# Optimization experiments

Measured on AMD Instinct MI355X. Metric: run time of the kernel, lower is better.

Reference implementation:

```python
import jax, jax.numpy as jnp
import numpy as np

N, E = 50000, 800000
DIN, DOUT = 256, 128
DH = 2 * DOUT  # hidden width of conv1


def setup_inputs() -> dict:
    key = jax.random.key(0)
    ks = jax.random.split(key, 9)
    x = jax.random.normal(ks[0], (N, DIN), dtype=jnp.float32)
    edge_index = jax.random.randint(ks[1], (2, E), 0, N, dtype=jnp.int64)
    edge_weight = jax.random.uniform(ks[2], (E,), dtype=jnp.float32)
    s1 = 1.0 / np.sqrt(DIN)
    s2 = 1.0 / np.sqrt(DH)
    W1 = jax.random.uniform(ks[3], (DIN, DH), minval=-s1, maxval=s1, dtype=jnp.float32)
    b1 = jnp.zeros((DH,), jnp.float32)
    Wmu = jax.random.uniform(ks[4], (DH, DOUT), minval=-s2, maxval=s2, dtype=jnp.float32)
    bmu = jnp.zeros((DOUT,), jnp.float32)
    Wls = jax.random.uniform(ks[5], (DH, DOUT), minval=-s2, maxval=s2, dtype=jnp.float32)
    bls = jnp.zeros((DOUT,), jnp.float32)
    return {"x": x, "edge_index": edge_index, "edge_weight": edge_weight,
            "W1": W1, "b1": b1, "Wmu": Wmu, "bmu": bmu, "Wls": Wls, "bls": bls}


def _gcn_layer(x, row, col, norm, W, b, n):
    # GCNConv: linear transform, then normalized scatter-add aggregation, then bias
    h = x @ W                                   # [N, Dout]
    msg = h[row] * norm[:, None]                # gather source feats, scale per-edge
    agg = jax.ops.segment_sum(msg, col, num_segments=n)  # scatter-add to targets
    return agg + b


def reference(x, edge_index, edge_weight, W1, b1, Wmu, bmu, Wls, bls):
    n = x.shape[0]
    row, col = edge_index[0], edge_index[1]
    # add self loops with weight 1 (PyG gcn_norm default, fill_value=1)
    loop = jnp.arange(n)
    row_f = jnp.concatenate([row, loop])
    col_f = jnp.concatenate([col, loop])
    ew = jnp.concatenate([edge_weight, jnp.ones((n,), x.dtype)])
    # symmetric normalization: deg computed over destination index
    deg = jax.ops.segment_sum(ew, col_f, num_segments=n)
    dinv = jnp.where(deg > 0, jax.lax.rsqrt(deg), 0.0)
    norm = dinv[row_f] * ew * dinv[col_f]       # cached=True -> same norm each layer
    h = jax.nn.relu(_gcn_layer(x, row_f, col_f, norm, W1, b1, n))
    mu = _gcn_layer(h, row_f, col_f, norm, Wmu, bmu, n)
    logstd = _gcn_layer(h, row_f, col_f, norm, Wls, bls, n)
    return mu, logstd
```

## Files before the change

### kernel.cpp

```cpp
#include <hip/hip_runtime.h>
#include <hip/hip_fp16.h>

#define THREADS 256
#define DEG_SHIFT 44
#define DEG_SCALE 16777216.0f
#define DEG_MASK  ((1ULL << DEG_SHIFT) - 1)

typedef __attribute__((ext_vector_type(8))) short bf16x8;
typedef __attribute__((ext_vector_type(4))) float f32x4;
typedef __attribute__((ext_vector_type(8))) unsigned short u16x8;

__device__ inline float bf2f(unsigned short u) {
    union { unsigned int i; float f; } v; v.i = ((unsigned int)u) << 16; return v.f;
}
__device__ inline unsigned short f2bf(float f) {
    union { float f; unsigned int i; } v; v.f = f;
    unsigned int i = v.i;
    i += 0x7fff + ((i >> 16) & 1);
    return (unsigned short)(i >> 16);
}

__global__ void k_init(unsigned long long* __restrict__ packed, int n) {
    int i = blockIdx.x * THREADS + threadIdx.x;
    if (i < n) packed[i] = 0ULL;
}

__global__ void k_count(const int* __restrict__ dst, const float* __restrict__ ew,
                        unsigned long long* __restrict__ packed,
                        int* __restrict__ rank, int E) {
    int e = blockIdx.x * THREADS + threadIdx.x;
    if (e >= E) return;
    int c = dst[e];
    unsigned long long v = (1ULL << DEG_SHIFT) |
        (unsigned long long)(ew[e] * DEG_SCALE + 0.5f);
    unsigned long long old = atomicAdd(&packed[c], v);
    rank[e] = (int)(old >> DEG_SHIFT);
}

__global__ void k_unpack(const unsigned long long* __restrict__ packed,
                         int* __restrict__ counts, float* __restrict__ dinv, int n) {
    int i = blockIdx.x * THREADS + threadIdx.x;
    if (i >= n) return;
    unsigned long long p = packed[i];
    counts[i] = (int)(p >> DEG_SHIFT);
    float d = 1.0f + (float)(p & DEG_MASK) * (1.0f / DEG_SCALE);
    dinv[i] = rsqrtf(d);
}

__global__ void k_scan_part(const int* __restrict__ counts, int* __restrict__ offsets,
                            int* __restrict__ blocksum, int n) {
    __shared__ int s[THREADS];
    int i = blockIdx.x * THREADS + threadIdx.x;
    int v = (i < n) ? counts[i] : 0;
    s[threadIdx.x] = v;
    __syncthreads();
    for (int d = 1; d < THREADS; d <<= 1) {
        int t = (threadIdx.x >= d) ? s[threadIdx.x - d] : 0;
        __syncthreads();
        s[threadIdx.x] += t;
        __syncthreads();
    }
    if (i < n) offsets[i] = s[threadIdx.x] - v;
    if (threadIdx.x == THREADS - 1) blocksum[blockIdx.x] = s[THREADS - 1];
}

__global__ void k_scan_block(int* __restrict__ blocksum, int nb) {
    __shared__ int s[THREADS];
    int v = (threadIdx.x < nb) ? blocksum[threadIdx.x] : 0;
    s[threadIdx.x] = v;
    __syncthreads();
    for (int d = 1; d < THREADS; d <<= 1) {
        int t = (threadIdx.x >= d) ? s[threadIdx.x - d] : 0;
        __syncthreads();
        s[threadIdx.x] += t;
        __syncthreads();
    }
    if (threadIdx.x < nb) blocksum[threadIdx.x] = s[threadIdx.x] - v;
}

__global__ void k_scan_add(int* __restrict__ offsets, const int* __restrict__ blocksum,
                           const int* __restrict__ counts, int2* __restrict__ combo, int n) {
    int i = blockIdx.x * THREADS + threadIdx.x;
    if (i >= n) return;
    int o = offsets[i] + blocksum[blockIdx.x];
    offsets[i] = o;
    combo[i] = make_int2(o, counts[i]);
}

__global__ void k_fill(const int* __restrict__ ei, const float* __restrict__ ew,
                       const float* __restrict__ dinv, const int* __restrict__ offsets,
                       const int* __restrict__ rank, unsigned int* __restrict__ csr, int E) {
    int e = blockIdx.x * THREADS + threadIdx.x;
    if (e >= E) return;
    int r = ei[e];
    int c = ei[E + e];
    float nrm = dinv[r] * ew[e] * dinv[c];
    unsigned short h = __half_as_ushort(__float2half_rn(nrm));
    csr[offsets[c] + rank[e]] = ((unsigned int)r << 16) | h;
}

__global__ void k_cvt_w(const float* __restrict__ W1, const float* __restrict__ Wmu,
                        const float* __restrict__ Wls, const float* __restrict__ bmu,
                        const float* __restrict__ bls,
                        ushort* __restrict__ W1t, ushort* __restrict__ Wct,
                        float* __restrict__ bcat) {
    int n = blockIdx.x, k = threadIdx.x;
    if (n < 256) {
        W1t[n * 256 + k] = f2bf(W1[k * 256 + n]);
    } else if (n < 512) {
        int nn = n - 256;
        float v = (nn < 128) ? Wmu[k * 128 + nn] : Wls[k * 128 + (nn - 128)];
        Wct[nn * 256 + k] = f2bf(v);
    } else {
        bcat[k] = (k < 128) ? bmu[k] : bls[k - 128];
    }
}

template<int MODE>
__global__ __launch_bounds__(256) void k_agg(const ushort* __restrict__ fb,
        const int2* __restrict__ combo, const unsigned int* __restrict__ csr,
        const float* __restrict__ dinv, const float* __restrict__ bias,
        void* __restrict__ out, int n) {
    int slice = blockIdx.x & 7;
    int grp   = blockIdx.x >> 3;
    int wv = threadIdx.x >> 6, lane = threadIdx.x & 63;
    int n2 = lane >> 4;
    int g  = (lane >> 2) & 3;
    int c  = lane & 3;
    int col0 = slice * 32;

    float b8[8];
    {
        const float4* bp = (const float4*)(bias + col0 + c * 8);
        float4 b0 = bp[0], b1 = bp[1];
        b8[0] = b0.x; b8[1] = b0.y; b8[2] = b0.z; b8[3] = b0.w;
        b8[4] = b1.x; b8[5] = b1.y; b8[6] = b1.z; b8[7] = b1.w;
    }

    int node = grp * 16 + wv * 4 + n2;
    bool valid = node < n;
    int nid = valid ? node : 0;
    int2 oc = combo[nid];
    int off = oc.x, cnt = valid ? oc.y : 0;
    float di = dinv[nid];

    float acc[8] = {};
    if (g == 0 && valid) {
        u16x8 u = *(const u16x8*)(fb + (size_t)nid * 256 + col0 + c * 8);
        float s = di * di;
        #pragma unroll
        for (int k = 0; k < 8; k++) acc[k] = s * bf2f(u[k]);
    }

    int cmax = cnt;
    cmax = max(cmax, __shfl_xor(cmax, 16));
    cmax = max(cmax, __shfl_xor(cmax, 32));

    const unsigned int* row = csr + off;
    for (int e0 = 0; e0 < cmax; e0 += 4) {
        int e = e0 + g;
        unsigned int m = (e < cnt) ? row[e] : 0u;
        int src = (int)(m >> 16);
        float w = __half2float(__ushort_as_half((unsigned short)(m & 0xffffu)));
        u16x8 u = *(const u16x8*)(fb + (size_t)src * 256 + col0 + c * 8);
        #pragma unroll
        for (int k = 0; k < 8; k++) acc[k] += w * bf2f(u[k]);
    }

    #pragma unroll
    for (int k = 0; k < 8; k++) acc[k] += __shfl_xor(acc[k], 4);
    #pragma unroll
    for (int k = 0; k < 8; k++) acc[k] += __shfl_xor(acc[k], 8);

    if (g == 0 && valid) {
        #pragma unroll
        for (int k = 0; k < 8; k++) acc[k] += b8[k];
        if (MODE == 0) {
            u16x8 o;
            #pragma unroll
            for (int k = 0; k < 8; k++) o[k] = f2bf(fmaxf(acc[k], 0.f));
            *(u16x8*)((ushort*)out + (size_t)node * 256 + col0 + c * 8) = o;
        } else {
            float* mu = (float*)out;
            float* dst = (slice < 4)
                ? mu + (size_t)node * 128 + col0 + c * 8
                : mu + (size_t)n * 128 + (size_t)node * 128 + (col0 - 128) + c * 8;
            float4* d4 = (float4*)dst;
            float4 o0, o1;
            o0.x = acc[0]; o0.y = acc[1]; o0.z = acc[2]; o0.w = acc[3];
            o1.x = acc[4]; o1.y = acc[5]; o1.z = acc[6]; o1.w = acc[7];
            d4[0] = o0; d4[1] = o1;
        }
    }
}

#define LDT 40
template<int AF32>
__global__ __launch_bounds__(256) void k_gemm(const void* __restrict__ Ain,
        const ushort* __restrict__ Bt, ushort* __restrict__ C, int M) {
    __shared__ ushort As[128 * LDT];
    __shared__ ushort Bs[128 * LDT];
    const float*  Af = (const float*)Ain;
    const ushort* Ab = (const ushort*)Ain;
    int tid = threadIdx.x;
    int lane = tid & 63, wave = tid >> 6;
    int row0 = blockIdx.y * 128, col0 = blockIdx.x * 128;
    int mw = (wave >> 1) * 64, nw = (wave & 1) * 64;
    int lr = lane & 15, lq = lane >> 4;
    f32x4 acc[4][4] = {};
    for (int k0 = 0; k0 < 256; k0 += 32) {
        #pragma unroll
        for (int i = 0; i < 2; i++) {
            int cc = tid + i * 256;
            int r = cc >> 2, q = cc & 3;
            int gr = row0 + r;
            int4 av = make_int4(0, 0, 0, 0);
            if (gr < M) {
                if (AF32) {
                    const float* p = Af + (size_t)gr * 256 + k0 + q * 8;
                    float4 lo = *(const float4*)p;
                    float4 hi = *(const float4*)(p + 4);
                    ushort* u = (ushort*)&av;
                    u[0] = f2bf(lo.x); u[1] = f2bf(lo.y);
                    u[2] = f2bf(lo.z); u[3] = f2bf(lo.w);
                    u[4] = f2bf(hi.x); u[5] = f2bf(hi.y);
                    u[6] = f2bf(hi.z); u[7] = f2bf(hi.w);
                } else {
                    av = *(const int4*)(Ab + (size_t)gr * 256 + k0 + q * 8);
                }
            }
            *(int4*)(&As[r * LDT + q * 8]) = av;
            int4 bv = *(const int4*)(Bt + (size_t)(col0 + r) * 256 + k0 + q * 8);
            *(int4*)(&Bs[r * LDT + q * 8]) = bv;
        }
        __syncthreads();
        bf16x8 af[4], bfr[4];
        #pragma unroll
        for (int mi = 0; mi < 4; mi++)
            af[mi] = *(const bf16x8*)(&As[(mw + mi * 16 + lr) * LDT + lq * 8]);
        #pragma unroll
        for (int ni = 0; ni < 4; ni++)
            bfr[ni] = *(const bf16x8*)(&Bs[(nw + ni * 16 + lr) * LDT + lq * 8]);
        #pragma unroll
        for (int mi = 0; mi < 4; mi++)
            #pragma unroll
            for (int ni = 0; ni < 4; ni++)
                acc[mi][ni] = __builtin_amdgcn_mfma_f32_16x16x32_bf16(
                    af[mi], bfr[ni], acc[mi][ni], 0, 0, 0);
        __syncthreads();
    }
    #pragma unroll
    for (int mi = 0; mi < 4; mi++)
        #pragma unroll
        for (int ni = 0; ni < 4; ni++)
            #pragma unroll
            for (int r = 0; r < 4; r++) {
                int grow = row0 + mw + mi * 16 + lq * 4 + r;
                int gcol = col0 + nw + ni * 16 + lr;
                if (grow < M) C[(size_t)grow * 256 + gcol] = f2bf(acc[mi][ni][r]);
            }
}

extern "C" void kernel_launch(void* const* d_in, const int* in_sizes, int n_in,
                              void* d_out, int out_size, void* d_ws, size_t ws_size,
                              hipStream_t stream) {
    const float* x   = (const float*)d_in[0];
    const int*   ei  = (const int*)d_in[1];
    const float* ew  = (const float*)d_in[2];
    const float* W1  = (const float*)d_in[3];
    const float* b1  = (const float*)d_in[4];
    const float* Wmu = (const float*)d_in[5];
    const float* bmu = (const float*)d_in[6];
    const float* Wls = (const float*)d_in[7];
    const float* bls = (const float*)d_in[8];

    const int DIN = 256;
    const int N = in_sizes[0] / DIN;
    const int E = in_sizes[2];

    unsigned long long* packed = (unsigned long long*)d_ws;
    int*   counts   = (int*)(packed + N);
    int*   offsets  = counts + N;
    float* dinv     = (float*)(offsets + N);
    int2*  combo    = (int2*)(dinv + N);
    int*   blocksum = (int*)(combo + N);
    int*   rank     = blocksum + 256;
    unsigned int* csr = (unsigned int*)(rank + E);
    ushort* xw      = (ushort*)(csr + E);
    ushort* hb      = xw + (size_t)N * 256;
    ushort* hw      = hb + (size_t)N * 256;
    ushort* W1t     = hw + (size_t)N * 256;
    ushort* Wct     = W1t + 256 * 256;
    float*  bcat    = (float*)(Wct + 256 * 256);

    int gN = (N + THREADS - 1) / THREADS;
    int gE = (E + THREADS - 1) / THREADS;

    k_init<<<gN, THREADS, 0, stream>>>(packed, N);
    k_count<<<gE, THREADS, 0, stream>>>(ei + E, ew, packed, rank, E);
    k_unpack<<<gN, THREADS, 0, stream>>>(packed, counts, dinv, N);

    k_scan_part<<<gN, THREADS, 0, stream>>>(counts, offsets, blocksum, N);
    k_scan_block<<<1, THREADS, 0, stream>>>(blocksum, gN);
    k_scan_add<<<gN, THREADS, 0, stream>>>(offsets, blocksum, counts, combo, N);

    k_fill<<<gE, THREADS, 0, stream>>>(ei, ew, dinv, offsets, rank, csr, E);

    k_cvt_w<<<513, THREADS, 0, stream>>>(W1, Wmu, Wls, bmu, bls, W1t, Wct, bcat);

    int gAgg = 8 * ((N + 15) / 16);
    dim3 ggrid(2, (N + 127) / 128);

    k_gemm<1><<<ggrid, 256, 0, stream>>>(x, W1t, xw, N);
    k_agg<0><<<gAgg, THREADS, 0, stream>>>(xw, combo, csr, dinv, b1, hb, N);

    k_gemm<0><<<ggrid, 256, 0, stream>>>(hb, Wct, hw, N);
    k_agg<1><<<gAgg, THREADS, 0, stream>>>(hw, combo, csr, dinv, bcat, d_out, N);
}
```

Before: 396.6 us.

## Pad CSR rows to multiples of four and aggregate one node per wave

The exclusive scan now rounds each node's edge count up to a multiple of four, so every CSR row starts 16-byte aligned and can be read with a single uint4 load. The aggregation kernel is remapped so each wave handles one node over a 64-column slice: eight edge groups each process four preloaded edges, then a tail loop covers rows with more than 32 edges. Per-node loop divergence across wave lanes goes away, and the CSR index fetch becomes vectorized. In exchange, waves with fewer than 32 edges still issue masked gathers of row 0, cross-lane reductions grow to three shuffle stages, and the workspace grows to hold the padding.

```diff
diff --git a/kernel.cpp b/kernel.cpp
--- a/kernel.cpp
+++ b/kernel.cpp
@@ -51,7 +51,7 @@
                             int* __restrict__ blocksum, int n) {
     __shared__ int s[THREADS];
     int i = blockIdx.x * THREADS + threadIdx.x;
-    int v = (i < n) ? counts[i] : 0;
+    int v = (i < n) ? ((counts[i] + 3) & ~3) : 0;
     s[threadIdx.x] = v;
     __syncthreads();
     for (int d = 1; d < THREADS; d <<= 1) {
@@ -121,29 +121,23 @@
         const int2* __restrict__ combo, const unsigned int* __restrict__ csr,
         const float* __restrict__ dinv, const float* __restrict__ bias,
         void* __restrict__ out, int n) {
-    int slice = blockIdx.x & 7;
-    int grp   = blockIdx.x >> 3;
+    int slice = blockIdx.x & 3;
+    int grp   = blockIdx.x >> 2;
     int wv = threadIdx.x >> 6, lane = threadIdx.x & 63;
-    int n2 = lane >> 4;
-    int g  = (lane >> 2) & 3;
-    int c  = lane & 3;
-    int col0 = slice * 32;
-
-    float b8[8];
-    {
-        const float4* bp = (const float4*)(bias + col0 + c * 8);
-        float4 b0 = bp[0], b1 = bp[1];
-        b8[0] = b0.x; b8[1] = b0.y; b8[2] = b0.z; b8[3] = b0.w;
-        b8[4] = b1.x; b8[5] = b1.y; b8[6] = b1.z; b8[7] = b1.w;
-    }
-
-    int node = grp * 16 + wv * 4 + n2;
+    int g = lane >> 3;
+    int c = lane & 7;
+    int col0 = slice * 64;
+
+    int node = grp * 4 + wv;
     bool valid = node < n;
     int nid = valid ? node : 0;
     int2 oc = combo[nid];
     int off = oc.x, cnt = valid ? oc.y : 0;
     float di = dinv[nid];
 
+    const unsigned int* row = csr + off;
+    uint4 q = *(const uint4*)(row + 4 * g);
+
     float acc[8] = {};
     if (g == 0 && valid) {
         u16x8 u = *(const u16x8*)(fb + (size_t)nid * 256 + col0 + c * 8);
@@ -152,29 +146,44 @@
         for (int k = 0; k < 8; k++) acc[k] = s * bf2f(u[k]);
     }
 
-    int cmax = cnt;
-    cmax = max(cmax, __shfl_xor(cmax, 16));
-    cmax = max(cmax, __shfl_xor(cmax, 32));
-
-    const unsigned int* row = csr + off;
-    for (int e0 = 0; e0 < cmax; e0 += 4) {
-        int e = e0 + g;
-        unsigned int m = (e < cnt) ? row[e] : 0u;
-        int src = (int)(m >> 16);
-        float w = __half2float(__ushort_as_half((unsigned short)(m & 0xffffu)));
-        u16x8 u = *(const u16x8*)(fb + (size_t)src * 256 + col0 + c * 8);
-        #pragma unroll
-        for (int k = 0; k < 8; k++) acc[k] += w * bf2f(u[k]);
-    }
-
-    #pragma unroll
-    for (int k = 0; k < 8; k++) acc[k] += __shfl_xor(acc[k], 4);
+    {
+        unsigned int mm[4] = { q.x, q.y, q.z, q.w };
+        #pragma unroll
+        for (int j = 0; j < 4; j++) {
+            int e = 4 * g + j;
+            unsigned int m = (e < cnt) ? mm[j] : 0u;
+            int src = (int)(m >> 16);
+            float w = __half2float(__ushort_as_half((unsigned short)(m & 0xffffu)));
+            u16x8 u = *(const u16x8*)(fb + (size_t)src * 256 + col0 + c * 8);
+            #pragma unroll
+            for (int k = 0; k < 8; k++) acc[k] += w * bf2f(u[k]);
+        }
+    }
+    if (cnt > 32) {
+        for (int e0 = 32; e0 < cnt; e0 += 8) {
+            int e = e0 + g;
+            unsigned int m = (e < cnt) ? row[e] : 0u;
+            int src = (int)(m >> 16);
+            float w = __half2float(__ushort_as_half((unsigned short)(m & 0xffffu)));
+            u16x8 u = *(const u16x8*)(fb + (size_t)src * 256 + col0 + c * 8);
+            #pragma unroll
+            for (int k = 0; k < 8; k++) acc[k] += w * bf2f(u[k]);
+        }
+    }
+
     #pragma unroll
     for (int k = 0; k < 8; k++) acc[k] += __shfl_xor(acc[k], 8);
+    #pragma unroll
+    for (int k = 0; k < 8; k++) acc[k] += __shfl_xor(acc[k], 16);
+    #pragma unroll
+    for (int k = 0; k < 8; k++) acc[k] += __shfl_xor(acc[k], 32);
 
     if (g == 0 && valid) {
-        #pragma unroll
-        for (int k = 0; k < 8; k++) acc[k] += b8[k];
+        const float4* bp = (const float4*)(bias + col0 + c * 8);
+        float4 b0 = bp[0], b1 = bp[1];
+        float bb[8] = { b0.x, b0.y, b0.z, b0.w, b1.x, b1.y, b1.z, b1.w };
+        #pragma unroll
+        for (int k = 0; k < 8; k++) acc[k] += bb[k];
         if (MODE == 0) {
             u16x8 o;
             #pragma unroll
@@ -182,7 +191,7 @@
             *(u16x8*)((ushort*)out + (size_t)node * 256 + col0 + c * 8) = o;
         } else {
             float* mu = (float*)out;
-            float* dst = (slice < 4)
+            float* dst = (slice < 2)
                 ? mu + (size_t)node * 128 + col0 + c * 8
                 : mu + (size_t)n * 128 + (size_t)node * 128 + (col0 - 128) + c * 8;
             float4* d4 = (float4*)dst;
@@ -286,7 +295,7 @@
     int*   blocksum = (int*)(combo + N);
     int*   rank     = blocksum + 256;
     unsigned int* csr = (unsigned int*)(rank + E);
-    ushort* xw      = (ushort*)(csr + E);
+    ushort* xw      = (ushort*)(csr + E + 4 * N + 32);
     ushort* hb      = xw + (size_t)N * 256;
     ushort* hw      = hb + (size_t)N * 256;
     ushort* W1t     = hw + (size_t)N * 256;
@@ -308,7 +317,7 @@
 
     k_cvt_w<<<513, THREADS, 0, stream>>>(W1, Wmu, Wls, bmu, bls, W1t, Wct, bcat);
 
-    int gAgg = 8 * ((N + 15) / 16);
+    int gAgg = 4 * ((N + 3) / 4);
     dim3 ggrid(2, (N + 127) / 128);
 
     k_gemm<1><<<ggrid, 256, 0, stream>>>(x, W1t, xw, N);
```

Measured after the change: 435.9 us. +9.9%, slower.

## Store intermediate features in column-sliced layout and fuse degree unpack into scan

Applied to the files above, without the earlier changes.

Intermediate bf16 feature buffers are stored as eight 32-column slices, each contiguous over all nodes, so each aggregation block's gather touches a compact region per slice. The goal is better L2 locality for the random neighbour gathers. The GEMMs now read and write this sliced layout, and the degree unpack kernel is merged into the scan's first pass, which removes one launch. Nontemporal loads for CSR entries and nontemporal stores for outputs are added, and the bias load moves to after the reduction. The GEMM's scalar bf16 output stores now land at a stride of 32 elements across column slices, which may lower write coalescing.

```diff
diff --git a/kernel.cpp b/kernel.cpp
--- a/kernel.cpp
+++ b/kernel.cpp
@@ -9,6 +9,8 @@
 typedef __attribute__((ext_vector_type(8))) short bf16x8;
 typedef __attribute__((ext_vector_type(4))) float f32x4;
 typedef __attribute__((ext_vector_type(8))) unsigned short u16x8;
+typedef __attribute__((ext_vector_type(4))) unsigned int u32x4;
+typedef __attribute__((ext_vector_type(4))) float fx4;
 
 __device__ inline float bf2f(unsigned short u) {
     union { unsigned int i; float f; } v; v.i = ((unsigned int)u) << 16; return v.f;
@@ -37,21 +39,19 @@
     rank[e] = (int)(old >> DEG_SHIFT);
 }
 
-__global__ void k_unpack(const unsigned long long* __restrict__ packed,
-                         int* __restrict__ counts, float* __restrict__ dinv, int n) {
-    int i = blockIdx.x * THREADS + threadIdx.x;
-    if (i >= n) return;
-    unsigned long long p = packed[i];
-    counts[i] = (int)(p >> DEG_SHIFT);
-    float d = 1.0f + (float)(p & DEG_MASK) * (1.0f / DEG_SCALE);
-    dinv[i] = rsqrtf(d);
-}
-
-__global__ void k_scan_part(const int* __restrict__ counts, int* __restrict__ offsets,
-                            int* __restrict__ blocksum, int n) {
+__global__ void k_scan_part(const unsigned long long* __restrict__ packed,
+                            int* __restrict__ counts, float* __restrict__ dinv,
+                            int* __restrict__ offsets, int* __restrict__ blocksum, int n) {
     __shared__ int s[THREADS];
     int i = blockIdx.x * THREADS + threadIdx.x;
-    int v = (i < n) ? counts[i] : 0;
+    int v = 0;
+    if (i < n) {
+        unsigned long long p = packed[i];
+        v = (int)(p >> DEG_SHIFT);
+        counts[i] = v;
+        float d = 1.0f + (float)(p & DEG_MASK) * (1.0f / DEG_SCALE);
+        dinv[i] = rsqrtf(d);
+    }
     s[threadIdx.x] = v;
     __syncthreads();
     for (int d = 1; d < THREADS; d <<= 1) {
@@ -120,7 +120,7 @@
 __global__ __launch_bounds__(256) void k_agg(const ushort* __restrict__ fb,
         const int2* __restrict__ combo, const unsigned int* __restrict__ csr,
         const float* __restrict__ dinv, const float* __restrict__ bias,
-        void* __restrict__ out, int n) {
+        void* __restrict__ out, int n, int sstr) {
     int slice = blockIdx.x & 7;
     int grp   = blockIdx.x >> 3;
     int wv = threadIdx.x >> 6, lane = threadIdx.x & 63;
@@ -128,14 +128,7 @@
     int g  = (lane >> 2) & 3;
     int c  = lane & 3;
     int col0 = slice * 32;
-
-    float b8[8];
-    {
-        const float4* bp = (const float4*)(bias + col0 + c * 8);
-        float4 b0 = bp[0], b1 = bp[1];
-        b8[0] = b0.x; b8[1] = b0.y; b8[2] = b0.z; b8[3] = b0.w;
-        b8[4] = b1.x; b8[5] = b1.y; b8[6] = b1.z; b8[7] = b1.w;
-    }
+    const ushort* ft = fb + (size_t)slice * sstr;
 
     int node = grp * 16 + wv * 4 + n2;
     bool valid = node < n;
@@ -146,7 +139,7 @@
 
     float acc[8] = {};
     if (g == 0 && valid) {
-        u16x8 u = *(const u16x8*)(fb + (size_t)nid * 256 + col0 + c * 8);
+        u16x8 u = *(const u16x8*)(ft + (size_t)nid * 32 + c * 8);
         float s = di * di;
         #pragma unroll
         for (int k = 0; k < 8; k++) acc[k] = s * bf2f(u[k]);
@@ -159,10 +152,11 @@
     const unsigned int* row = csr + off;
     for (int e0 = 0; e0 < cmax; e0 += 4) {
         int e = e0 + g;
-        unsigned int m = (e < cnt) ? row[e] : 0u;
+        unsigned int m = 0u;
+        if (e < cnt) m = __builtin_nontemporal_load(row + e);
         int src = (int)(m >> 16);
         float w = __half2float(__ushort_as_half((unsigned short)(m & 0xffffu)));
-        u16x8 u = *(const u16x8*)(fb + (size_t)src * 256 + col0 + c * 8);
+        u16x8 u = *(const u16x8*)(ft + (size_t)src * 32 + c * 8);
         #pragma unroll
         for (int k = 0; k < 8; k++) acc[k] += w * bf2f(u[k]);
     }
@@ -173,23 +167,28 @@
     for (int k = 0; k < 8; k++) acc[k] += __shfl_xor(acc[k], 8);
 
     if (g == 0 && valid) {
-        #pragma unroll
-        for (int k = 0; k < 8; k++) acc[k] += b8[k];
+        const float4* bp = (const float4*)(bias + col0 + c * 8);
+        float4 b0 = bp[0], b1 = bp[1];
+        float bb[8] = { b0.x, b0.y, b0.z, b0.w, b1.x, b1.y, b1.z, b1.w };
+        #pragma unroll
+        for (int k = 0; k < 8; k++) acc[k] += bb[k];
         if (MODE == 0) {
             u16x8 o;
             #pragma unroll
             for (int k = 0; k < 8; k++) o[k] = f2bf(fmaxf(acc[k], 0.f));
-            *(u16x8*)((ushort*)out + (size_t)node * 256 + col0 + c * 8) = o;
+            u32x4 ov = *(u32x4*)&o;
+            __builtin_nontemporal_store(ov,
+                (u32x4*)((ushort*)out + (size_t)slice * sstr + (size_t)node * 32 + c * 8));
         } else {
             float* mu = (float*)out;
             float* dst = (slice < 4)
                 ? mu + (size_t)node * 128 + col0 + c * 8
                 : mu + (size_t)n * 128 + (size_t)node * 128 + (col0 - 128) + c * 8;
-            float4* d4 = (float4*)dst;
-            float4 o0, o1;
+            fx4 o0, o1;
             o0.x = acc[0]; o0.y = acc[1]; o0.z = acc[2]; o0.w = acc[3];
             o1.x = acc[4]; o1.y = acc[5]; o1.z = acc[6]; o1.w = acc[7];
-            d4[0] = o0; d4[1] = o1;
+            __builtin_nontemporal_store(o0, (fx4*)dst);
+            __builtin_nontemporal_store(o1, (fx4*)dst + 1);
         }
     }
 }
@@ -197,7 +196,7 @@
 #define LDT 40
 template<int AF32>
 __global__ __launch_bounds__(256) void k_gemm(const void* __restrict__ Ain,
-        const ushort* __restrict__ Bt, ushort* __restrict__ C, int M) {
+        const ushort* __restrict__ Bt, ushort* __restrict__ C, int M, int sstr) {
     __shared__ ushort As[128 * LDT];
     __shared__ ushort Bs[128 * LDT];
     const float*  Af = (const float*)Ain;
@@ -226,7 +225,8 @@
                     u[4] = f2bf(hi.x); u[5] = f2bf(hi.y);
                     u[6] = f2bf(hi.z); u[7] = f2bf(hi.w);
                 } else {
-                    av = *(const int4*)(Ab + (size_t)gr * 256 + k0 + q * 8);
+                    av = *(const int4*)(Ab + (size_t)(k0 >> 5) * sstr
+                                        + (size_t)gr * 32 + q * 8);
                 }
             }
             *(int4*)(&As[r * LDT + q * 8]) = av;
@@ -257,7 +257,9 @@
             for (int r = 0; r < 4; r++) {
                 int grow = row0 + mw + mi * 16 + lq * 4 + r;
                 int gcol = col0 + nw + ni * 16 + lr;
-                if (grow < M) C[(size_t)grow * 256 + gcol] = f2bf(acc[mi][ni][r]);
+                if (grow < M)
+                    C[(size_t)(gcol >> 5) * sstr + (size_t)grow * 32 + (gcol & 31)]
+                        = f2bf(acc[mi][ni][r]);
             }
 }
 
@@ -277,6 +279,7 @@
     const int DIN = 256;
     const int N = in_sizes[0] / DIN;
     const int E = in_sizes[2];
+    const int SSTR = N * 32;
 
     unsigned long long* packed = (unsigned long long*)d_ws;
     int*   counts   = (int*)(packed + N);
@@ -286,7 +289,7 @@
     int*   blocksum = (int*)(combo + N);
     int*   rank     = blocksum + 256;
     unsigned int* csr = (unsigned int*)(rank + E);
-    ushort* xw      = (ushort*)(csr + E);
+    ushort* xw      = (ushort*)(csr + E + 32);
     ushort* hb      = xw + (size_t)N * 256;
     ushort* hw      = hb + (size_t)N * 256;
     ushort* W1t     = hw + (size_t)N * 256;
@@ -298,9 +301,8 @@
 
     k_init<<<gN, THREADS, 0, stream>>>(packed, N);
     k_count<<<gE, THREADS, 0, stream>>>(ei + E, ew, packed, rank, E);
-    k_unpack<<<gN, THREADS, 0, stream>>>(packed, counts, dinv, N);
-
-    k_scan_part<<<gN, THREADS, 0, stream>>>(counts, offsets, blocksum, N);
+
+    k_scan_part<<<gN, THREADS, 0, stream>>>(packed, counts, dinv, offsets, blocksum, N);
     k_scan_block<<<1, THREADS, 0, stream>>>(blocksum, gN);
     k_scan_add<<<gN, THREADS, 0, stream>>>(offsets, blocksum, counts, combo, N);
 
@@ -311,9 +313,9 @@
     int gAgg = 8 * ((N + 15) / 16);
     dim3 ggrid(2, (N + 127) / 128);
 
-    k_gemm<1><<<ggrid, 256, 0, stream>>>(x, W1t, xw, N);
-    k_agg<0><<<gAgg, THREADS, 0, stream>>>(xw, combo, csr, dinv, b1, hb, N);
-
-    k_gemm<0><<<ggrid, 256, 0, stream>>>(hb, Wct, hw, N);
-    k_agg<1><<<gAgg, THREADS, 0, stream>>>(hw, combo, csr, dinv, bcat, d_out, N);
-}
+    k_gemm<1><<<ggrid, 256, 0, stream>>>(x, W1t, xw, N, SSTR);
+    k_agg<0><<<gAgg, THREADS, 0, stream>>>(xw, combo, csr, dinv, b1, hb, N, SSTR);
+
+    k_gemm<0><<<ggrid, 256, 0, stream>>>(hb, Wct, hw, N, SSTR);
+    k_agg<1><<<gAgg, THREADS, 0, stream>>>(hw, combo, csr, dinv, bcat, d_out, N, SSTR);
+}
```

After: 439.3 us. +10.8%, slower.
